# Performance work log

Measured on AMD Instinct MI355X. Metric: run time of the kernel, lower is better.

Reference implementation:

```python
import jax, jax.numpy as jnp
import numpy as np

E, C, L, B = 8, 128, 1024, 32
FB = L // 2 + 1        # 513 freq bins
HD = 2 * FB            # 1026 hidden dim


def setup_inputs() -> dict:
    key = jax.random.key(0)
    ks = jax.random.split(key, 8)
    return {
        "X_time": jax.random.normal(ks[0], (B, C, L), jnp.float32),
        "bound_params": jax.random.normal(ks[1], (E - 1,), jnp.float32),
        "W1r": jax.random.normal(ks[2], (E, HD, FB), jnp.float32) * 0.1,
        "W1i": jax.random.normal(ks[3], (E, HD, FB), jnp.float32) * 0.1,
        "b1r": jnp.zeros((E, HD), jnp.float32),
        "b1i": jnp.zeros((E, HD), jnp.float32),
        "W2r": jax.random.normal(ks[4], (E, FB, HD), jnp.float32) * 0.1,
        "W2i": jax.random.normal(ks[5], (E, FB, HD), jnp.float32) * 0.1,
        "b2r": jnp.zeros((E, FB), jnp.float32),
        "b2i": jnp.zeros((E, FB), jnp.float32),
        "gate_W": jax.random.normal(ks[6], (E, FB), jnp.float32) * 0.1,
        "gate_b": jnp.zeros((E,), jnp.float32),
    }


def reference(X_time, bound_params, W1r, W1i, b1r, b1i, W2r, W2i, b2r, b2i, gate_W, gate_b):
    Bx, Cx, Lx = X_time.shape
    fb = Lx // 2 + 1
    e = W1r.shape[0]

    Xf = jnp.fft.rfft(X_time, axis=-1)                     # [B,C,FB] complex

    # learnable frequency-band binary masks
    raw = jax.nn.sigmoid(bound_params)
    bounds = jnp.sort(jnp.concatenate([jnp.zeros(1, raw.dtype), raw, jnp.ones(1, raw.dtype)]))
    idx = (bounds * (fb - 1)).astype(jnp.int32)
    starts = idx[:e]
    ends = jnp.concatenate([idx[1:e], jnp.array([fb], jnp.int32)])
    pos = jnp.arange(fb)
    masks = ((pos[None, :] >= starts[:, None]) & (pos[None, :] < ends[:, None])).astype(X_time.dtype)  # [E,FB]

    # masked spectra per expert, split into real/imag: [E,B,C,FB]
    m = masks[:, None, None, :]
    xr = Xf.real * m
    xi = Xf.imag * m

    # expert layer 1: complex linear (W [E,HD,FB]) + complex ReLU
    hr = jnp.einsum('ehf,ebcf->ebch', W1r, xr) - jnp.einsum('ehf,ebcf->ebch', W1i, xi) + b1r[:, None, None, :]
    hi = jnp.einsum('ehf,ebcf->ebch', W1r, xi) + jnp.einsum('ehf,ebcf->ebch', W1i, xr) + b1i[:, None, None, :]
    hr = jax.nn.relu(hr)
    hi = jax.nn.relu(hi)

    # expert layer 2: complex linear (W [E,FB,HD]) -> [E,B,C,FB]
    yr = jnp.einsum('efh,ebch->ebcf', W2r, hr) - jnp.einsum('efh,ebch->ebcf', W2i, hi) + b2r[:, None, None, :]
    yi = jnp.einsum('efh,ebch->ebcf', W2r, hi) + jnp.einsum('efh,ebch->ebcf', W2i, hr) + b2i[:, None, None, :]

    # gate: mean |Xf| over channels -> linear -> softmax over experts
    mag = jnp.mean(jnp.abs(Xf), axis=1)                    # [B,FB]
    gate = jax.nn.softmax(mag @ gate_W.T + gate_b, axis=-1)  # [B,E]

    comb_r = jnp.einsum('ebcf,be->bcf', yr, gate)
    comb_i = jnp.einsum('ebcf,be->bcf', yi, gate)
    return jnp.fft.irfft(jax.lax.complex(comb_r, comb_i), n=Lx, axis=-1)
```

## Files before the change

### kernel.cpp

```cpp
#include <hip/hip_runtime.h>
#include <hip/hip_bf16.h>
#include <math.h>

typedef __hip_bfloat16 bf16;
typedef __attribute__((ext_vector_type(8))) short short8;
typedef __attribute__((ext_vector_type(4))) short short4v;
typedef __attribute__((ext_vector_type(4))) float f32x4;

#define FB 513
#define HD 1026
#define NN 1024
#define MR 4096
#define NE 8
#define BATCH 32

#define XINT_LD 1056
#define FINV_LD 1088
#define HP_LD   2080
#define B1_ROWS 2176
#define KCAT    16640
#define PLANE   ((size_t)MR * XINT_LD)
#define MAG_LD  520

__device__ __forceinline__ void gload16(const void* g, void* l) {
    __builtin_amdgcn_global_load_lds((const __attribute__((address_space(1))) void*)g,
                                     (__attribute__((address_space(3))) void*)l, 16, 0, 0);
}
__device__ __forceinline__ bf16 f2b(float v) { return __float2bfloat16(v); }
__device__ __forceinline__ unsigned short f2bu(float v) {
    bf16 b = __float2bfloat16(v);
    return *reinterpret_cast<unsigned short*>(&b);
}
__device__ __forceinline__ float bu2f(unsigned short u) {
    return __uint_as_float(((unsigned)u) << 16);
}
__device__ __forceinline__ unsigned pack2(float a, float b) {
    return (unsigned)f2bu(a) | ((unsigned)f2bu(b) << 16);
}

__device__ __forceinline__ void xcd_swizzle(int* px, int* py) {
    int gx = gridDim.x;
    int orig = blockIdx.x + gx * blockIdx.y;
    int q = (gx * gridDim.y) >> 3;
    int wg = (orig & 7) * q + (orig >> 3);
    *px = wg % gx;
    *py = wg / gx;
}

__global__ void prep_kernel(const float* __restrict__ bp, int* __restrict__ se) {
    if (threadIdx.x == 0 && blockIdx.x == 0) {
        float b[9];
        b[0] = 0.0f; b[8] = 1.0f;
        for (int i = 0; i < 7; i++) b[i + 1] = 1.0f / (1.0f + expf(-bp[i]));
        for (int i = 1; i < 9; i++) { float v = b[i]; int j = i - 1;
            while (j >= 0 && b[j] > v) { b[j + 1] = b[j]; j--; } b[j + 1] = v; }
        int idx[9];
        for (int i = 0; i < 9; i++) idx[i] = (int)(b[i] * (float)(FB - 1));
        for (int e = 0; e < NE; e++) {
            se[2 * e] = idx[e];
            se[2 * e + 1] = (e < NE - 1) ? idx[e + 1] : FB;
        }
    }
}

#define N_FF  (1056L * 1024)
#define N_FI  (1024L * FINV_LD)
#define N_B1P ((long)NE * B1_ROWS * (XINT_LD / 2))
#define N_B2T ((long)KCAT * (FINV_LD / 2))
#define N_XP  ((long)MR * NN / 2)
#define N_PREP (N_FF + N_FI + N_B1P + N_B2T + N_XP)

__global__ void prep_bulk(const float* __restrict__ W1r, const float* __restrict__ W1i,
                          const float* __restrict__ W2r, const float* __restrict__ W2i,
                          const float* __restrict__ X, const int* __restrict__ se,
                          bf16* __restrict__ Ffwd, bf16* __restrict__ Finv,
                          bf16* __restrict__ B1, bf16* __restrict__ B2t,
                          bf16* __restrict__ Xb) {
    long i = (long)blockIdx.x * 256 + threadIdx.x;
    const float TWO_PI = 6.283185307179586f;
    if (i < N_FF) {
        int n = (int)(i >> 10), t = (int)(i & (NN - 1));
        float v = 0.0f;
        if (n < 2 * FB) {
            int f = n >> 1, k = (f * t) & (NN - 1);
            float s, c; sincosf(TWO_PI * (float)k / (float)NN, &s, &c);
            v = (n & 1) ? -s : c;
        }
        Ffwd[i] = f2b(v);
        return;
    }
    i -= N_FF;
    if (i < N_FI) {
        int t = (int)(i / FINV_LD), k = (int)(i % FINV_LD);
        float v = 0.0f;
        if (k < 2 * FB) {
            int f = k >> 1, kk = (f * t) & (NN - 1);
            float s, c; sincosf(TWO_PI * (float)kk / (float)NN, &s, &c);
            float cf = (f == 0 || f == FB - 1) ? 1.0f : 2.0f;
            float sc = cf * (1.0f / (float)NN);
            v = (k & 1) ? -s * sc : c * sc;
        }
        Finv[i] = f2b(v);
        return;
    }
    i -= N_FI;
    if (i < N_B1P) {
        int f = (int)(i % (XINT_LD / 2));
        long t = i / (XINT_LD / 2);
        int n = (int)(t % B1_ROWS);
        int e = (int)(t / B1_ROWS);
        float ve = 0.0f, vo = 0.0f;
        if (n < 2 * HD && f < FB && f >= se[2 * e] && f < se[2 * e + 1]) {
            int hi_part = (n >= HD);
            int h = hi_part ? n - HD : n;
            long wi = ((long)e * HD + h) * FB + f;
            float wr = W1r[wi], wim = W1i[wi];
            ve = hi_part ? wim : wr;
            vo = hi_part ? wr : -wim;
        }
        *(unsigned*)(B1 + ((size_t)(e * B1_ROWS + n)) * XINT_LD + 2 * f) = pack2(ve, vo);
        return;
    }
    i -= N_B1P;
    if (i < N_B2T) {
        int fp = (int)(i % (FINV_LD / 2));
        int k = (int)(i / (FINV_LD / 2));
        int e = k / HP_LD, kk2 = k % HP_LD;
        float vr = 0.0f, vi_ = 0.0f;
        if (fp < FB && kk2 < 2 * HD) {
            int hi_part = (kk2 >= HD);
            int h = hi_part ? kk2 - HD : kk2;
            long wi = ((long)e * FB + fp) * HD + h;
            float wr = W2r[wi], wim = W2i[wi];
            vr  = hi_part ? -wim : wr;
            vi_ = hi_part ? wr : wim;
        }
        *(unsigned*)(B2t + (size_t)k * FINV_LD + 2 * fp) = pack2(vr, vi_);
        return;
    }
    i -= N_B2T;
    if (i < N_XP) {
        float2 v = ((const float2*)X)[i];
        *(unsigned*)(Xb + 2 * i) = pack2(v.x, v.y);
    }
}

__global__ void mag_kernel(const bf16* __restrict__ Xint, float* __restrict__ magp) {
    int b = blockIdx.x, g = blockIdx.y, t = threadIdx.x;
    float acc[3] = {0.0f, 0.0f, 0.0f};
    const bf16* base = Xint + ((size_t)b * 128 + g * 16) * XINT_LD;
    for (int c = 0; c < 16; c++) {
        const bf16* row = base + (size_t)c * XINT_LD;
#pragma unroll
        for (int kk = 0; kk < 3; kk++) {
            int f = t + 256 * kk;
            if (f < FB) {
                float xr = __bfloat162float(row[2 * f]);
                float xi = __bfloat162float(row[2 * f + 1]);
                acc[kk] += sqrtf(xr * xr + xi * xi);
            }
        }
    }
#pragma unroll
    for (int kk = 0; kk < 3; kk++) {
        int f = t + 256 * kk;
        if (f < FB) magp[((size_t)b * 8 + g) * MAG_LD + f] = acc[kk];
    }
}

__global__ void gate_bias_kernel(const float* __restrict__ magp, const float* __restrict__ gW,
                                 const float* __restrict__ gb, const float* __restrict__ b2r,
                                 const float* __restrict__ b2i, float* __restrict__ gate,
                                 float* __restrict__ biasCs) {
    __shared__ float sred[256];
    __shared__ float sg[8];
    int b = blockIdx.x, tid = threadIdx.x;
    int e = tid & 7, j = tid >> 3;
    float acc = 0.0f;
    for (int f = j; f < FB; f += 32) {
        float m = 0.0f;
#pragma unroll
        for (int g = 0; g < 8; g++) m += magp[((size_t)b * 8 + g) * MAG_LD + f];
        acc += m * (1.0f / 128.0f) * gW[e * FB + f];
    }
    sred[tid] = acc;
    __syncthreads();
    if (tid < 64) {
        float a = sred[tid] + sred[tid + 64] + sred[tid + 128] + sred[tid + 192];
        a += __shfl_xor(a, 8); a += __shfl_xor(a, 16); a += __shfl_xor(a, 32);
        float logit = a + gb[e];
        float mx = logit;
        mx = fmaxf(mx, __shfl_xor(mx, 1)); mx = fmaxf(mx, __shfl_xor(mx, 2)); mx = fmaxf(mx, __shfl_xor(mx, 4));
        float ex = expf(logit - mx);
        float sum = ex;
        sum += __shfl_xor(sum, 1); sum += __shfl_xor(sum, 2); sum += __shfl_xor(sum, 4);
        if (tid < 8) { float g_ = ex / sum; sg[tid] = g_; gate[b * NE + tid] = g_; }
    }
    __syncthreads();
    for (int c = tid; c < XINT_LD; c += 256) {
        float v = 0.0f;
        if (c < 2 * FB) {
            int f = c >> 1;
            const float* bb = (c & 1) ? b2i : b2r;
#pragma unroll
            for (int ee = 0; ee < NE; ee++) v += sg[ee] * bb[ee * FB + f];
            float cf = (f == 0 || f == FB - 1) ? 1.0f : 2.0f;
            v *= cf * (1.0f / (float)NN);
        }
        biasCs[b * XINT_LD + c] = v;
    }
}

__global__ void biasT_kernel(const float* __restrict__ biasCs, const bf16* __restrict__ Ffwd,
                             float* __restrict__ biasT) {
    int t = blockIdx.x * 256 + threadIdx.x;
    int b = blockIdx.y;
    float s = 0.0f;
    for (int c = 0; c < 2 * FB; c++)
        s += biasCs[b * XINT_LD + c] * __bfloat162float(Ffwd[(size_t)c * NN + t]);
    biasT[b * NN + t] = s;
}

__global__ void reduce_f32(const float* __restrict__ planes, bf16* __restrict__ outp) {
    long idx = (long)blockIdx.x * 256 + threadIdx.x;
    if (idx >= (long)MR * (XINT_LD / 4)) return;
    int c4 = (int)(idx % (XINT_LD / 4));
    long r = idx / (XINT_LD / 4);
    int c0 = c4 * 4;
    size_t base = (size_t)r * XINT_LD + c0;
    float4 a = *(const float4*)(planes + base);
    float4 b = *(const float4*)(planes + PLANE + base);
    float s[4] = {a.x + b.x, a.y + b.y, a.z + b.z, a.w + b.w};
    short4v o;
#pragma unroll
    for (int j = 0; j < 4; j++) o[j] = (short)f2bu((c0 + j < 2 * FB) ? s[j] : 0.0f);
    *(short4v*)(outp + base) = o;
}

__global__ void reduce_out4(const bf16* __restrict__ planes, const float* __restrict__ biasT,
                            float* __restrict__ out) {
    long idx = (long)blockIdx.x * 256 + threadIdx.x;
    if (idx >= (long)MR * NN / 8) return;
    size_t base = (size_t)idx * 8;
    long r = base >> 10;
    int t = (int)(base & (NN - 1));
    float s[8] = {};
#pragma unroll
    for (int z = 0; z < 4; z++) {
        short8 v = *(const short8*)(planes + (size_t)z * MR * NN + base);
#pragma unroll
        for (int j = 0; j < 8; j++) s[j] += bu2f((unsigned short)v[j]);
    }
    const float* bT = biasT + (r >> 7) * NN + t;
    float4 o0 = {s[0] + bT[0], s[1] + bT[1], s[2] + bT[2], s[3] + bT[3]};
    float4 o1 = {s[4] + bT[4], s[5] + bT[5], s[6] + bT[6], s[7] + bT[7]};
    *(float4*)(out + base) = o0;
    *(float4*)(out + base + 4) = o1;
}

template <int EPI>
__global__ void gemm_mfma(const bf16* __restrict__ A, int lda,
                          const bf16* __restrict__ B, int ldb, size_t zBstride,
                          void* __restrict__ Cv, int ldc, size_t zCoff,
                          int N, int K, int kPerZ,
                          const int* __restrict__ se2,
                          const float* __restrict__ biasR, const float* __restrict__ biasI,
                          int zBias, const float* __restrict__ gate8) {
    __shared__ bf16 As[128 * 32];
    __shared__ bf16 Bs[128 * 32];
    int tid = threadIdx.x;
    int zz = blockIdx.z;
    int bx, by;
    xcd_swizzle(&bx, &by);
    int row0 = by * 128, col0 = bx * 128;
    const bf16* Bz = B + (size_t)zz * zBstride;

    int kS, kE;
    if (EPI == 1) { int s = se2[2 * zz], e = se2[2 * zz + 1]; kS = (2 * s) & ~31; kE = (2 * e + 31) & ~31; }
    else          { kS = zz * kPerZ; kE = min(K, kS + kPerZ); }

    f32x4 acc[4][4] = {};

    int lane = tid & 63, wid = tid >> 6;
    int wrB = (wid >> 1) << 6, wcB = (wid & 1) << 6;
    int lr = lane & 15, lk = (lane >> 4) << 3;

    int r_a = tid >> 2, c_a = (tid & 3) << 3;
    int r_b = (tid + 256) >> 2, c_b = ((tid + 256) & 3) << 3;

    for (int kt = kS; kt < kE; kt += 32) {
        gload16(A + (size_t)(row0 + r_a) * lda + kt + c_a, &As[(size_t)tid * 8]);
        gload16(A + (size_t)(row0 + r_b) * lda + kt + c_b, &As[((size_t)tid + 256) * 8]);
        gload16(Bz + (size_t)(col0 + r_a) * ldb + kt + c_a, &Bs[(size_t)tid * 8]);
        gload16(Bz + (size_t)(col0 + r_b) * ldb + kt + c_b, &Bs[((size_t)tid + 256) * 8]);
        __syncthreads();
        short8 av[4], bv[4];
#pragma unroll
        for (int m = 0; m < 4; m++)
            av[m] = *(const short8*)&As[(wrB + m * 16 + lr) * 32 + lk];
#pragma unroll
        for (int n = 0; n < 4; n++)
            bv[n] = *(const short8*)&Bs[(wcB + n * 16 + lr) * 32 + lk];
#pragma unroll
        for (int m = 0; m < 4; m++)
#pragma unroll
            for (int n = 0; n < 4; n++)
                acc[m][n] = __builtin_amdgcn_mfma_f32_16x16x32_bf16(av[m], bv[n], acc[m][n], 0, 0, 0);
        __syncthreads();
    }

    int r0 = row0 + wrB + ((lane >> 4) << 2);
    int c0i = col0 + wcB + (lane & 15);
    float g = (EPI == 1) ? gate8[(row0 >> 7) * NE + zz] : 0.0f;

#pragma unroll
    for (int m = 0; m < 4; m++)
#pragma unroll
        for (int n = 0; n < 4; n++) {
            int c = c0i + n * 16;
            if (c >= N) continue;
#pragma unroll
            for (int j = 0; j < 4; j++) {
                int r = r0 + m * 16 + j;
                float v = acc[m][n][j];
                if (EPI == 1) {
                    v += (c < HD) ? biasR[zz * zBias + c] : biasI[zz * zBias + c - HD];
                    v = fmaxf(v, 0.0f) * g;
                    ((bf16*)Cv + (size_t)zz * zCoff)[(size_t)r * ldc + c] = f2b(v);
                } else {
                    ((float*)Cv + (size_t)zz * zCoff)[(size_t)r * ldc + c] = v;
                }
            }
        }
}

__device__ __forceinline__ void stage_half(const bf16* gbase, int ld, int kt,
                                           bf16* ldsBase, int tid) {
#pragma unroll
    for (int j = 0; j < 2; j++) {
        int r = j * 64 + (tid >> 3);
        int sc = ((tid & 7) ^ ((tid >> 3) & 7)) * 8;
        gload16(gbase + (size_t)r * ld + kt + sc, ldsBase + j * 4096 + tid * 8);
    }
}

#define MF(a, b, c) __builtin_amdgcn_mfma_f32_16x16x32_bf16(a, b, c, 0, 0, 0)
#define RD(off) (*(const short8*)(bc + (off)))

#define PHASE_MFMA(FM)                                                        \
    {                                                                         \
        short8 aa0 = RD(aBase + (FM) * 1024 + cb0);                           \
        short8 aa1 = RD(aBase + (FM) * 1024 + cb1);                           \
        short8 ab0 = RD(aBase + (FM + 1) * 1024 + cb0);                       \
        short8 ab1 = RD(aBase + (FM + 1) * 1024 + cb1);                       \
        __builtin_amdgcn_s_setprio(1);                                        \
        acc[FM][0] = MF(aa0, b0[0], acc[FM][0]);                              \
        acc[FM][0] = MF(aa1, b1[0], acc[FM][0]);                              \
        acc[FM][1] = MF(aa0, b0[1], acc[FM][1]);                              \
        acc[FM][1] = MF(aa1, b1[1], acc[FM][1]);                              \
        acc[FM][2] = MF(aa0, b0[2], acc[FM][2]);                              \
        acc[FM][2] = MF(aa1, b1[2], acc[FM][2]);                              \
        acc[FM][3] = MF(aa0, b0[3], acc[FM][3]);                              \
        acc[FM][3] = MF(aa1, b1[3], acc[FM][3]);                              \
        acc[FM + 1][0] = MF(ab0, b0[0], acc[FM + 1][0]);                      \
        acc[FM + 1][0] = MF(ab1, b1[0], acc[FM + 1][0]);                      \
        acc[FM + 1][1] = MF(ab0, b0[1], acc[FM + 1][1]);                      \
        acc[FM + 1][1] = MF(ab1, b1[1], acc[FM + 1][1]);                      \
        acc[FM + 1][2] = MF(ab0, b0[2], acc[FM + 1][2]);                      \
        acc[FM + 1][2] = MF(ab1, b1[2], acc[FM + 1][2]);                      \
        acc[FM + 1][3] = MF(ab0, b0[3], acc[FM + 1][3]);                      \
        acc[FM + 1][3] = MF(ab1, b1[3], acc[FM + 1][3]);                      \
        __builtin_amdgcn_s_setprio(0);                                        \
        __builtin_amdgcn_sched_barrier(0);                                    \
        __builtin_amdgcn_s_barrier();                                         \
    }

template <int SWZ>
__global__ __launch_bounds__(512, 2) void gemm8p(
        const bf16* __restrict__ A, int lda, const bf16* __restrict__ B, int ldb,
        bf16* __restrict__ C, int ldc, size_t zCoff,
        int tilesPerZ, int totTiles, int gx) {
    __shared__ bf16 sm[65536];
    int tid = threadIdx.x;
    int id = blockIdx.x;
    int bx, by, z;
    if (SWZ == 1) {
        int by_z = (id & 7) * 8 + (id >> 5);
        bx = (id >> 3) & 3;
        z = by_z >> 4;
        by = by_z & 15;
    } else {
        bx = id % gx; by = id / gx; z = 0;
    }
    int row0 = by * 256, col0 = bx * 256;
    int t0 = z * tilesPerZ;
    int nt = min(tilesPerZ, totTiles - t0);
    int kS = t0 * 64;

    const bf16* Ab = A + (size_t)row0 * lda;
    const bf16* Bb = B + (size_t)col0 * ldb;

    stage_half(Ab, lda, kS, sm, tid);
    stage_half(Ab + (size_t)128 * lda, lda, kS, sm + 8192, tid);
    stage_half(Bb, ldb, kS, sm + 16384, tid);
    stage_half(Bb + (size_t)128 * ldb, ldb, kS, sm + 24576, tid);

    f32x4 acc[8][4] = {};

    int l = tid & 63, w = tid >> 6;
    int wm = w >> 2, wn = w & 3;
    int lr = l & 15, lk4 = l >> 4;
    int swz = lr & 7;
    int cb0 = ((lk4) ^ swz) * 8;
    int cb1 = ((4 + lk4) ^ swz) * 8;
    int aBaseR = wm * 8192 + lr * 64;
    int bBaseR = 16384 + (wn >> 1) * 8192 + (wn & 1) * 4096 + lr * 64;

    for (int t = 0; t < nt; ++t) {
        const int cur = t & 1;
        const bf16* bc = sm + cur * 32768;
        bf16* bufN = sm + (cur ^ 1) * 32768;
        int aBase = aBaseR, bBase = bBaseR;
        int ktn = kS + (t + 1) * 64;
        bool more = (t + 1) < nt;
        if (more) {
            stage_half(Ab, lda, ktn, bufN, tid);
            stage_half(Ab + (size_t)128 * lda, lda, ktn, bufN + 8192, tid);
            asm volatile("s_waitcnt vmcnt(4)" ::: "memory");
        } else {
            asm volatile("s_waitcnt vmcnt(0)" ::: "memory");
        }
        __builtin_amdgcn_s_barrier();
        __builtin_amdgcn_sched_barrier(0);
        short8 b0[4], b1[4];
#pragma unroll
        for (int n = 0; n < 4; n++) {
            b0[n] = RD(bBase + n * 1024 + cb0);
            b1[n] = RD(bBase + n * 1024 + cb1);
        }
        PHASE_MFMA(0)
        if (more) {
            stage_half(Bb, ldb, ktn, bufN + 16384, tid);
            stage_half(Bb + (size_t)128 * ldb, ldb, ktn, bufN + 24576, tid);
        }
        PHASE_MFMA(2)
        PHASE_MFMA(4)
        PHASE_MFMA(6)
    }

    bf16* Cp = C + (size_t)z * zCoff;
    int rb = row0 + wm * 128 + lk4 * 4;
    int cbase = col0 + wn * 64 + lr;
#pragma unroll
    for (int fm = 0; fm < 8; fm++)
#pragma unroll
        for (int n = 0; n < 4; n++)
#pragma unroll
            for (int j = 0; j < 4; j++)
                Cp[(size_t)(rb + fm * 16 + j) * ldc + cbase + n * 16] = f2b(acc[fm][n][j]);
}

extern "C" void kernel_launch(void* const* d_in, const int* in_sizes, int n_in,
                              void* d_out, int out_size, void* d_ws, size_t ws_size,
                              hipStream_t stream) {
    const float* X   = (const float*)d_in[0];
    const float* bp  = (const float*)d_in[1];
    const float* W1r = (const float*)d_in[2];
    const float* W1i = (const float*)d_in[3];
    const float* b1r = (const float*)d_in[4];
    const float* b1i = (const float*)d_in[5];
    const float* W2r = (const float*)d_in[6];
    const float* W2i = (const float*)d_in[7];
    const float* b2r = (const float*)d_in[8];
    const float* b2i = (const float*)d_in[9];
    const float* gW  = (const float*)d_in[10];
    const float* gb  = (const float*)d_in[11];
    float* out = (float*)d_out;

    const size_t SZH = (size_t)MR * HP_LD * 2;

    char* p = (char*)d_ws;
    auto alloc = [&](size_t bytes) -> char* {
        char* r = p; p += (bytes + 255) & ~255ULL; return r;
    };
    int*   se     = (int*)alloc(64 * 4);
    float* magp   = (float*)alloc((size_t)BATCH * 8 * MAG_LD * 4);
    float* gate   = (float*)alloc((size_t)BATCH * NE * 4);
    float* biasCs = (float*)alloc((size_t)BATCH * XINT_LD * 4);
    float* biasT  = (float*)alloc((size_t)BATCH * NN * 4);
    bf16*  Ffwd   = (bf16*)alloc(1056 * 1024 * 2);
    bf16*  Finv   = (bf16*)alloc((size_t)NN * FINV_LD * 2);
    bf16*  B1     = (bf16*)alloc((size_t)NE * B1_ROWS * XINT_LD * 2);
    bf16*  B2t    = (bf16*)alloc((size_t)KCAT * FINV_LD * 2);
    bf16*  Xint   = (bf16*)alloc(PLANE * 2);
    char*  planes = alloc(2 * PLANE * 4);
    bf16*  Hp     = (bf16*)alloc(8 * SZH);
    float* planesF = (float*)planes;
    bf16*  planesB = (bf16*)planes;
    bf16*  B2inv  = (bf16*)B1;
    bf16*  Xb     = (bf16*)((char*)Hp + 8 * SZH - (size_t)MR * NN * 2);

    prep_kernel<<<1, 64, 0, stream>>>(bp, se);
    prep_bulk<<<(unsigned)((N_PREP + 255) / 256), 256, 0, stream>>>(
        W1r, W1i, W2r, W2i, X, se, Ffwd, Finv, B1, B2t, Xb);

    gemm_mfma<3><<<dim3(9, 32, 2), 256, 0, stream>>>(
        Xb, NN, Ffwd, NN, 0, planesF, XINT_LD, PLANE,
        1056, NN, 512, nullptr, nullptr, nullptr, 0, nullptr);
    reduce_f32<<<(unsigned)(((size_t)MR * (XINT_LD / 4) + 255) / 256), 256, 0, stream>>>(
        planesF, Xint);

    mag_kernel<<<dim3(BATCH, 8), 256, 0, stream>>>(Xint, magp);
    gate_bias_kernel<<<BATCH, 256, 0, stream>>>(magp, gW, gb, b2r, b2i, gate, biasCs);
    biasT_kernel<<<dim3(4, BATCH), 256, 0, stream>>>(biasCs, Ffwd, biasT);

    gemm_mfma<1><<<dim3(17, 32, 8), 256, 0, stream>>>(
        Xint, XINT_LD, B1, XINT_LD, (size_t)B1_ROWS * XINT_LD,
        Hp, NE * HP_LD, HP_LD, 2 * HD, 0, 0,
        se, b1r, b1i, HD, gate);

    gemm8p<0><<<260, 512, 0, stream>>>(
        Finv, FINV_LD, B2t, FINV_LD, B2inv, KCAT, 0, 17, 17, 65);

    gemm8p<1><<<256, 512, 0, stream>>>(
        Hp, KCAT, B2inv, KCAT, planesB, NN, (size_t)MR * NN, 65, 260, 4);

    reduce_out4<<<(unsigned)(((size_t)MR * NN / 8 + 255) / 256), 256, 0, stream>>>(
        planesB, biasT, out);
}
```

Before: 470.6 us.

## Replace split-K forward DFT GEMM and reduce with gemm8p; tile-transpose W2 packing

The forward DFT now runs on the gemm8p kernel, which writes bf16 Xint directly. This replaces the split-K gemm_mfma pass that produced two fp32 planes and the separate reduce_f32 pass, so it removes the fp32 intermediate traffic and one launch. Xint and Ffwd padding grow to 1280 columns/rows to fit the new tiling, which adds some padded work in the layer-1 GEMM. W2 packing moves out of prep_bulk into a shared-memory tiled transpose kernel with coalesced reads and vector stores.

```diff
diff --git a/kernel.cpp b/kernel.cpp
--- a/kernel.cpp
+++ b/kernel.cpp
@@ -4,7 +4,6 @@
 
 typedef __hip_bfloat16 bf16;
 typedef __attribute__((ext_vector_type(8))) short short8;
-typedef __attribute__((ext_vector_type(4))) short short4v;
 typedef __attribute__((ext_vector_type(4))) float f32x4;
 
 #define FB 513
@@ -14,13 +13,14 @@
 #define NE 8
 #define BATCH 32
 
-#define XINT_LD 1056
+#define XINT_LD 1280
+#define BIAS_LD 1056
 #define FINV_LD 1088
 #define HP_LD   2080
 #define B1_ROWS 2176
 #define KCAT    16640
-#define PLANE   ((size_t)MR * XINT_LD)
 #define MAG_LD  520
+#define FF_ROWS 1280
 
 __device__ __forceinline__ void gload16(const void* g, void* l) {
     __builtin_amdgcn_global_load_lds((const __attribute__((address_space(1))) void*)g,
@@ -63,19 +63,16 @@
     }
 }
 
-#define N_FF  (1056L * 1024)
+#define N_FF  ((long)FF_ROWS * NN)
 #define N_FI  (1024L * FINV_LD)
 #define N_B1P ((long)NE * B1_ROWS * (XINT_LD / 2))
-#define N_B2T ((long)KCAT * (FINV_LD / 2))
 #define N_XP  ((long)MR * NN / 2)
-#define N_PREP (N_FF + N_FI + N_B1P + N_B2T + N_XP)
+#define N_PREP (N_FF + N_FI + N_B1P + N_XP)
 
 __global__ void prep_bulk(const float* __restrict__ W1r, const float* __restrict__ W1i,
-                          const float* __restrict__ W2r, const float* __restrict__ W2i,
                           const float* __restrict__ X, const int* __restrict__ se,
                           bf16* __restrict__ Ffwd, bf16* __restrict__ Finv,
-                          bf16* __restrict__ B1, bf16* __restrict__ B2t,
-                          bf16* __restrict__ Xb) {
+                          bf16* __restrict__ B1, bf16* __restrict__ Xb) {
     long i = (long)blockIdx.x * 256 + threadIdx.x;
     const float TWO_PI = 6.283185307179586f;
     if (i < N_FF) {
@@ -122,26 +119,54 @@
         return;
     }
     i -= N_B1P;
-    if (i < N_B2T) {
-        int fp = (int)(i % (FINV_LD / 2));
-        int k = (int)(i / (FINV_LD / 2));
-        int e = k / HP_LD, kk2 = k % HP_LD;
-        float vr = 0.0f, vi_ = 0.0f;
-        if (fp < FB && kk2 < 2 * HD) {
-            int hi_part = (kk2 >= HD);
-            int h = hi_part ? kk2 - HD : kk2;
-            long wi = ((long)e * FB + fp) * HD + h;
-            float wr = W2r[wi], wim = W2i[wi];
-            vr  = hi_part ? -wim : wr;
-            vi_ = hi_part ? wr : wim;
-        }
-        *(unsigned*)(B2t + (size_t)k * FINV_LD + 2 * fp) = pack2(vr, vi_);
-        return;
-    }
-    i -= N_B2T;
     if (i < N_XP) {
         float2 v = ((const float2*)X)[i];
         *(unsigned*)(Xb + 2 * i) = pack2(v.x, v.y);
+    }
+}
+
+__global__ void pack_B2t(const float* __restrict__ W2r, const float* __restrict__ W2i,
+                         bf16* __restrict__ B2t) {
+    __shared__ float sR[64][65], sI[64][65];
+    int e = blockIdx.z;
+    int f0 = blockIdx.x * 64;
+    int h0 = blockIdx.y * 64;
+    int tid = threadIdx.x;
+#pragma unroll
+    for (int rep = 0; rep < 16; rep++) {
+        int idx = tid + rep * 256;
+        int fl = idx >> 6, hl = idx & 63;
+        int f = f0 + fl, h = h0 + hl;
+        bool ok = (f < FB) && (h < HD);
+        size_t wi = ((size_t)e * FB + f) * HD + h;
+        sR[fl][hl] = ok ? W2r[wi] : 0.0f;
+        sI[fl][hl] = ok ? W2i[wi] : 0.0f;
+    }
+    __syncthreads();
+#pragma unroll
+    for (int rep = 0; rep < 4; rep++) {
+        int idx = tid + rep * 256;
+        int hl = idx >> 4, ch = idx & 15;
+        int h = h0 + hl;
+        int c0 = 2 * f0 + ch * 8;
+        if (c0 >= FINV_LD) continue;
+        short8 lo, hi;
+#pragma unroll
+        for (int j = 0; j < 4; j++) {
+            int fl = ch * 4 + j;
+            float wr = sR[fl][hl], wim = sI[fl][hl];
+            lo[2 * j]     = (short)f2bu(wr);
+            lo[2 * j + 1] = (short)f2bu(wim);
+            hi[2 * j]     = (short)f2bu(-wim);
+            hi[2 * j + 1] = (short)f2bu(wr);
+        }
+        if (h < HD) {
+            *(short8*)(B2t + ((size_t)e * HP_LD + h) * FINV_LD + c0) = lo;
+            *(short8*)(B2t + ((size_t)e * HP_LD + HD + h) * FINV_LD + c0) = hi;
+        } else if (HD + h < HP_LD) {
+            short8 z = {};
+            *(short8*)(B2t + ((size_t)e * HP_LD + HD + h) * FINV_LD + c0) = z;
+        }
     }
 }
 
@@ -197,7 +222,7 @@
         if (tid < 8) { float g_ = ex / sum; sg[tid] = g_; gate[b * NE + tid] = g_; }
     }
     __syncthreads();
-    for (int c = tid; c < XINT_LD; c += 256) {
+    for (int c = tid; c < BIAS_LD; c += 256) {
         float v = 0.0f;
         if (c < 2 * FB) {
             int f = c >> 1;
@@ -207,7 +232,7 @@
             float cf = (f == 0 || f == FB - 1) ? 1.0f : 2.0f;
             v *= cf * (1.0f / (float)NN);
         }
-        biasCs[b * XINT_LD + c] = v;
+        biasCs[b * BIAS_LD + c] = v;
     }
 }
 
@@ -217,24 +242,8 @@
     int b = blockIdx.y;
     float s = 0.0f;
     for (int c = 0; c < 2 * FB; c++)
-        s += biasCs[b * XINT_LD + c] * __bfloat162float(Ffwd[(size_t)c * NN + t]);
+        s += biasCs[b * BIAS_LD + c] * __bfloat162float(Ffwd[(size_t)c * NN + t]);
     biasT[b * NN + t] = s;
-}
-
-__global__ void reduce_f32(const float* __restrict__ planes, bf16* __restrict__ outp) {
-    long idx = (long)blockIdx.x * 256 + threadIdx.x;
-    if (idx >= (long)MR * (XINT_LD / 4)) return;
-    int c4 = (int)(idx % (XINT_LD / 4));
-    long r = idx / (XINT_LD / 4);
-    int c0 = c4 * 4;
-    size_t base = (size_t)r * XINT_LD + c0;
-    float4 a = *(const float4*)(planes + base);
-    float4 b = *(const float4*)(planes + PLANE + base);
-    float s[4] = {a.x + b.x, a.y + b.y, a.z + b.z, a.w + b.w};
-    short4v o;
-#pragma unroll
-    for (int j = 0; j < 4; j++) o[j] = (short)f2bu((c0 + j < 2 * FB) ? s[j] : 0.0f);
-    *(short4v*)(outp + base) = o;
 }
 
 __global__ void reduce_out4(const bf16* __restrict__ planes, const float* __restrict__ biasT,
@@ -486,29 +495,25 @@
     int*   se     = (int*)alloc(64 * 4);
     float* magp   = (float*)alloc((size_t)BATCH * 8 * MAG_LD * 4);
     float* gate   = (float*)alloc((size_t)BATCH * NE * 4);
-    float* biasCs = (float*)alloc((size_t)BATCH * XINT_LD * 4);
+    float* biasCs = (float*)alloc((size_t)BATCH * BIAS_LD * 4);
     float* biasT  = (float*)alloc((size_t)BATCH * NN * 4);
-    bf16*  Ffwd   = (bf16*)alloc(1056 * 1024 * 2);
+    bf16*  Ffwd   = (bf16*)alloc((size_t)FF_ROWS * NN * 2);
     bf16*  Finv   = (bf16*)alloc((size_t)NN * FINV_LD * 2);
     bf16*  B1     = (bf16*)alloc((size_t)NE * B1_ROWS * XINT_LD * 2);
     bf16*  B2t    = (bf16*)alloc((size_t)KCAT * FINV_LD * 2);
-    bf16*  Xint   = (bf16*)alloc(PLANE * 2);
-    char*  planes = alloc(2 * PLANE * 4);
+    bf16*  Xint   = (bf16*)alloc((size_t)MR * XINT_LD * 2);
+    bf16*  planesB = (bf16*)alloc(4 * (size_t)MR * NN * 2);
     bf16*  Hp     = (bf16*)alloc(8 * SZH);
-    float* planesF = (float*)planes;
-    bf16*  planesB = (bf16*)planes;
     bf16*  B2inv  = (bf16*)B1;
     bf16*  Xb     = (bf16*)((char*)Hp + 8 * SZH - (size_t)MR * NN * 2);
 
     prep_kernel<<<1, 64, 0, stream>>>(bp, se);
     prep_bulk<<<(unsigned)((N_PREP + 255) / 256), 256, 0, stream>>>(
-        W1r, W1i, W2r, W2i, X, se, Ffwd, Finv, B1, B2t, Xb);
-
-    gemm_mfma<3><<<dim3(9, 32, 2), 256, 0, stream>>>(
-        Xb, NN, Ffwd, NN, 0, planesF, XINT_LD, PLANE,
-        1056, NN, 512, nullptr, nullptr, nullptr, 0, nullptr);
-    reduce_f32<<<(unsigned)(((size_t)MR * (XINT_LD / 4) + 255) / 256), 256, 0, stream>>>(
-        planesF, Xint);
+        W1r, W1i, X, se, Ffwd, Finv, B1, Xb);
+    pack_B2t<<<dim3(9, 17, 8), 256, 0, stream>>>(W2r, W2i, B2t);
+
+    gemm8p<0><<<80, 512, 0, stream>>>(
+        Xb, NN, Ffwd, NN, Xint, XINT_LD, 0, 16, 16, 5);
 
     mag_kernel<<<dim3(BATCH, 8), 256, 0, stream>>>(Xint, magp);
     gate_bias_kernel<<<BATCH, 256, 0, stream>>>(magp, gW, gb, b2r, b2i, gate, biasCs);
@@ -516,7 +521,7 @@
 
     gemm_mfma<1><<<dim3(17, 32, 8), 256, 0, stream>>>(
         Xint, XINT_LD, B1, XINT_LD, (size_t)B1_ROWS * XINT_LD,
-        Hp, NE * HP_LD, HP_LD, 2 * HD, 0, 0,
+        Hp, KCAT, HP_LD, 2 * HD, 0, 0,
         se, b1r, b1i, HD, gate);
 
     gemm8p<0><<<260, 512, 0, stream>>>(
```

Result: faster. 415.5 us (-11.7%).
